# Kernel optimization log

Hardware: AMD Instinct MI355X
Metric: run time of the kernel (lower is better)

## Reference

```python
import jax, jax.numpy as jnp
import numpy as np

B, L, D, NH, NP = 8, 4096, 384, 8, 4


def setup_inputs() -> dict:
    key = jax.random.key(0)
    ks = jax.random.split(key, 16)
    s = 1.0 / np.sqrt(D)
    f32 = jnp.float32
    inp = {
        'query': jax.random.normal(ks[0], (B, L, D), f32),
        'key':   jax.random.normal(ks[1], (B, L, D), f32),
        'value': jax.random.normal(ks[2], (B, L, D), f32),
        # linear weights stored as [in, out]; x @ W + b
        'Wq': jax.random.normal(ks[3], (D, D), f32) * s,
        'bq': jnp.zeros((D,), f32),
        'Wk': jax.random.normal(ks[4], (D, D), f32) * s,
        'bk': jnp.zeros((D,), f32),
        'Wv': jax.random.normal(ks[5], (D, D), f32) * s,
        'bv': jnp.zeros((D,), f32),
        'Woff': jax.random.normal(ks[6], (D, NH * NP * 2), f32) * s,
        'boff': jnp.zeros((NH * NP * 2,), f32),
        'Wwt': jax.random.normal(ks[7], (D, NH * NP), f32) * s,
        'bwt': jnp.zeros((NH * NP,), f32),
        'Wo': jax.random.normal(ks[8], (D, D), f32) * s,
        'bo': jnp.zeros((D,), f32),
        'num_heads': NH,
        'n_points': NP,
    }
    return inp


def reference(query, key, value, Wq, bq, Wk, bk, Wv, bv, Woff, boff, Wwt, bwt, Wo, bo, num_heads, n_points):
    Bq, Lq, Dm = query.shape
    Lk = key.shape[1]
    Lv = value.shape[1]
    hd = Dm // num_heads
    h = w = int(round(np.sqrt(Lk)))  # original: feature_size = int(sqrt(Lk))

    q = query @ Wq + bq          # computed as in original (only its reshape is used via output path)
    k = key @ Wk + bk            # faithful: k_proj is computed but unused downstream
    v = value @ Wv + bv

    # offsets [B, nH, Lq, nP, 2] and softmax point weights [B, nH, Lq, nP]
    off = (query @ Woff + boff).reshape(Bq, Lq, num_heads, n_points, 2).transpose(0, 2, 1, 3, 4)
    wt = jax.nn.softmax((query @ Wwt + bwt).reshape(Bq, Lq, num_heads, n_points).transpose(0, 2, 1, 3), axis=-1)

    # reference grid: ref[...,0] = x (tiled over rows), ref[...,1] = y (repeated over cols)
    yy = jnp.linspace(0.0, 1.0, h)
    xx = jnp.linspace(0.0, 1.0, w)
    gy, gx = jnp.meshgrid(yy, xx, indexing='ij')
    ref = jnp.stack([gx.reshape(-1), gy.reshape(-1)], axis=-1)  # [L, 2]

    loc = jnp.clip(ref[None, None, :, None, :] + off, 0.0, 1.0)  # [B,nH,Lq,nP,2]
    # NOTE: faithful to source, which multiplies component 0 by (h-1) (its 'h' coord)
    ph = loc[..., 0] * (h - 1)   # row pixel coord, in [0, h-1]
    pw = loc[..., 1] * (w - 1)   # col pixel coord, in [0, w-1]

    y0 = jnp.floor(ph)
    x0 = jnp.floor(pw)
    wy = (ph - y0)[..., None]
    wx = (pw - x0)[..., None]
    y0i = y0.astype(jnp.int32)
    x0i = x0.astype(jnp.int32)
    y1i = jnp.minimum(y0i + 1, h - 1)
    x1i = jnp.minimum(x0i + 1, w - 1)

    vh = v.reshape(Bq, Lv, num_heads, hd).transpose(0, 2, 1, 3)  # [B,nH,Lv,hd]

    def gather(yi, xi):
        idx = (yi * w + xi).reshape(Bq, num_heads, Lq * n_points, 1)
        return jnp.take_along_axis(vh, idx, axis=2).reshape(Bq, num_heads, Lq, n_points, hd)

    # bilinear sample (align_corners=True; coords in-range so zero-padding never triggers)
    sampled = ((1 - wy) * ((1 - wx) * gather(y0i, x0i) + wx * gather(y0i, x1i))
               + wy * ((1 - wx) * gather(y1i, x0i) + wx * gather(y1i, x1i)))

    out = jnp.einsum('bhlp,bhlpd->bhld', wt, sampled)  # weighted point aggregation
    out = out.transpose(0, 2, 1, 3).reshape(Bq, Lq, Dm)
    return out @ Wo + bo  # dropout is identity in eval mode
```

## Files before the change

### kernel.cpp

```cpp
#include <hip/hip_runtime.h>
#include <hip/hip_bf16.h>
#include <stdint.h>

using bf16 = __hip_bfloat16;

typedef __attribute__((ext_vector_type(8))) short short8;
typedef __attribute__((ext_vector_type(4))) float float4v;

namespace {
constexpr int kL  = 4096;
constexpr int kD  = 384;
constexpr int kNP = 4;
constexpr int kHD = 48;
constexpr int kGW = 64;
constexpr int kM  = 32768;

constexpr size_t nValue = (size_t)kM * kD;
constexpr size_t nW     = (size_t)kD * kD;
constexpr size_t nWcat  = (size_t)kD * 96;

constexpr size_t oWvt  = 0;
constexpr size_t oWot  = oWvt  + nW * 2;
constexpr size_t oWcat = oWot  + nW * 2;
constexpr size_t oBcat = oWcat + nWcat * 4;
constexpr size_t oVB   = (oBcat + 96 * 4 + 255) & ~size_t(255);
constexpr size_t oProj = oVB   + nValue * 2;
constexpr size_t oAgg  = oProj + (size_t)kM * 96 * 4;
}

__device__ __forceinline__ void load_lds_16(const void* g, void* l) {
  __builtin_amdgcn_global_load_lds((const __attribute__((address_space(1))) void*)g,
                                   (__attribute__((address_space(3))) void*)l,
                                   16, 0, 0);
}

__device__ __forceinline__ short bf16bits(float f) {
  bf16 h = __float2bfloat16(f);
  return *reinterpret_cast<short*>(&h);
}

__global__ void prep_kernel(const float* __restrict__ Wv,
                            const float* __restrict__ Wo,
                            const float* __restrict__ Woff,
                            const float* __restrict__ Wwt,
                            const float* __restrict__ boff,
                            const float* __restrict__ bwt,
                            bf16* __restrict__ Wvt, bf16* __restrict__ Wot,
                            float* __restrict__ Wcat, float* __restrict__ bcat)
{
  size_t i = (size_t)blockIdx.x * 256 + threadIdx.x;
  if (i < nW) {
    const int n = (int)(i / kD), k = (int)(i % kD);
    Wvt[i] = __float2bfloat16(Wv[(size_t)k * kD + n]);
    return;
  }
  i -= nW;
  if (i < nW) {
    const int n = (int)(i / kD), k = (int)(i % kD);
    Wot[i] = __float2bfloat16(Wo[(size_t)k * kD + n]);
    return;
  }
  i -= nW;
  if (i < nWcat) {
    const int k = (int)(i / 96), n = (int)(i % 96);
    Wcat[i] = (n < 64) ? Woff[(size_t)k * 64 + n] : Wwt[(size_t)k * 32 + (n - 64)];
    return;
  }
  i -= nWcat;
  if (i < 96) bcat[i] = (i < 64) ? boff[i] : bwt[i - 64];
}

template<bool A_F32, bool OUT_BF16>
__global__ __launch_bounds__(256)
void mfma_gemm_kernel(const void* __restrict__ A, const bf16* __restrict__ Bt,
                      const float* __restrict__ bias, void* __restrict__ Cout)
{
  __shared__ __align__(16) bf16 sA[128 * 32];
  __shared__ __align__(16) bf16 sB[128 * 32];
  const int tid  = threadIdx.x;
  const int lane = tid & 63;
  const int wave = tid >> 6;
  const int bm = blockIdx.x / 3, bn = blockIdx.x % 3;
  const int m0 = bm * 128, n0 = bn * 128;
  const int wm = (wave >> 1) * 64, wn = (wave & 1) * 64;
  const int r16 = lane & 15, quad = lane >> 4;

  float4v acc[4][4];
  #pragma unroll
  for (int i = 0; i < 4; ++i)
    #pragma unroll
    for (int j = 0; j < 4; ++j) acc[i][j] = (float4v){0.f, 0.f, 0.f, 0.f};

  const int c0 = tid, c1 = tid + 256;

  for (int kt = 0; kt < 12; ++kt) {
    const int k0 = kt * 32;
    if (A_F32) {
      const float* Af = (const float*)A;
      #pragma unroll
      for (int r = 0; r < 2; ++r) {
        const int e = tid + r * 256;
        const int row = e >> 2, c = e & 3;
        const float* src = Af + (size_t)(m0 + row) * kD + k0 + c * 8;
        const float4 f0 = *(const float4*)src;
        const float4 f1 = *(const float4*)(src + 4);
        short8 hx;
        hx[0] = bf16bits(f0.x); hx[1] = bf16bits(f0.y);
        hx[2] = bf16bits(f0.z); hx[3] = bf16bits(f0.w);
        hx[4] = bf16bits(f1.x); hx[5] = bf16bits(f1.y);
        hx[6] = bf16bits(f1.z); hx[7] = bf16bits(f1.w);
        *(short8*)((char*)sA + e * 16) = hx;
      }
    } else {
      const bf16* Ab = (const bf16*)A;
      load_lds_16(Ab + (size_t)(m0 + (c0 >> 2)) * kD + k0 + (c0 & 3) * 8, (char*)sA + c0 * 16);
      load_lds_16(Ab + (size_t)(m0 + (c1 >> 2)) * kD + k0 + (c1 & 3) * 8, (char*)sA + c1 * 16);
    }
    load_lds_16(Bt + (size_t)(n0 + (c0 >> 2)) * kD + k0 + (c0 & 3) * 8, (char*)sB + c0 * 16);
    load_lds_16(Bt + (size_t)(n0 + (c1 >> 2)) * kD + k0 + (c1 & 3) * 8, (char*)sB + c1 * 16);
    __syncthreads();

    short8 av[4], bv[4];
    #pragma unroll
    for (int i = 0; i < 4; ++i)
      av[i] = *(const short8*)(sA + (wm + i * 16 + r16) * 32 + quad * 8);
    #pragma unroll
    for (int j = 0; j < 4; ++j)
      bv[j] = *(const short8*)(sB + (wn + j * 16 + r16) * 32 + quad * 8);
    #pragma unroll
    for (int i = 0; i < 4; ++i)
      #pragma unroll
      for (int j = 0; j < 4; ++j)
        acc[i][j] = __builtin_amdgcn_mfma_f32_16x16x32_bf16(av[i], bv[j], acc[i][j], 0, 0, 0);
    __syncthreads();
  }

  #pragma unroll
  for (int j = 0; j < 4; ++j) {
    const int col = n0 + wn + j * 16 + r16;
    const float bj = bias[col];
    #pragma unroll
    for (int i = 0; i < 4; ++i) {
      const int mbase = m0 + wm + i * 16 + quad * 4;
      #pragma unroll
      for (int r = 0; r < 4; ++r) {
        const float val = acc[i][j][r] + bj;
        if (OUT_BF16)
          ((bf16*)Cout)[(size_t)(mbase + r) * kD + col] = __float2bfloat16(val);
        else
          ((float*)Cout)[(size_t)(mbase + r) * kD + col] = val;
      }
    }
  }
}

__global__ __launch_bounds__(256)
void proj_gemm_kernel(const float* __restrict__ Q, const float* __restrict__ Wc,
                      const float* __restrict__ bc, float* __restrict__ proj)
{
  __shared__ float sA[32][68];
  __shared__ float sB[32][100];
  const int tid = threadIdx.x;
  const int m0  = blockIdx.x * 64;
  const int tm  = tid >> 4, tn = tid & 15;

  float acc[4][6] = {};

  for (int kt = 0; kt < 12; ++kt) {
    const int k0 = kt * 32;
    #pragma unroll
    for (int r = 0; r < 2; ++r) {
      const int e = tid + r * 256;
      const int m = e >> 3, kc = e & 7;
      const float4 f = *(const float4*)(Q + (size_t)(m0 + m) * kD + k0 + kc * 4);
      sA[kc * 4 + 0][m] = f.x;
      sA[kc * 4 + 1][m] = f.y;
      sA[kc * 4 + 2][m] = f.z;
      sA[kc * 4 + 3][m] = f.w;
    }
    #pragma unroll
    for (int r = 0; r < 6; ++r) {
      const int e = tid + r * 256;
      const int k = e / 48, n2 = (e % 48) * 2;
      *(float2*)(&sB[k][n2]) = *(const float2*)(Wc + (size_t)(k0 + k) * 96 + n2);
    }
    __syncthreads();
    #pragma unroll
    for (int k = 0; k < 32; ++k) {
      const float4 a  = *(const float4*)(&sA[k][tm * 4]);
      const float2 b0 = *(const float2*)(&sB[k][tn * 6]);
      const float2 b1 = *(const float2*)(&sB[k][tn * 6 + 2]);
      const float2 b2 = *(const float2*)(&sB[k][tn * 6 + 4]);
      const float av[4] = {a.x, a.y, a.z, a.w};
      const float bb[6] = {b0.x, b0.y, b1.x, b1.y, b2.x, b2.y};
      #pragma unroll
      for (int i = 0; i < 4; ++i)
        #pragma unroll
        for (int j = 0; j < 6; ++j)
          acc[i][j] += av[i] * bb[j];
    }
    __syncthreads();
  }

  #pragma unroll
  for (int j = 0; j < 6; ++j) {
    const int col = tn * 6 + j;
    const float bj = bc[col];
    #pragma unroll
    for (int i = 0; i < 4; ++i)
      proj[(size_t)(m0 + tm * 4 + i) * 96 + col] = acc[i][j] + bj;
  }
}

__global__ __launch_bounds__(384)
void sample_kernel(const float* __restrict__ proj, const bf16* __restrict__ v,
                   bf16* __restrict__ agg)
{
  const int b = blockIdx.x & 7;
  const int l = blockIdx.x >> 3;
  const int token = b * kL + l;
  const int t = threadIdx.x;

  __shared__ float sp[96];
  __shared__ int   sy0[32], sx0[32], sy1[32], sx1[32];
  __shared__ float swy[32], swx[32], swt[32];

  if (t < 96) sp[t] = proj[(size_t)token * 96 + t];
  __syncthreads();

  if (t < 32) {
    const float offx = sp[2 * t];
    const float offy = sp[2 * t + 1];
    const float refx = (float)(l % kGW) * (1.0f / 63.0f);
    const float refy = (float)(l / kGW) * (1.0f / 63.0f);
    const float locx = fminf(fmaxf(refx + offx, 0.f), 1.f);
    const float locy = fminf(fmaxf(refy + offy, 0.f), 1.f);
    const float ph = locx * 63.0f;
    const float pw = locy * 63.0f;
    const float fy = floorf(ph), fx = floorf(pw);
    const int y0 = (int)fy, x0 = (int)fx;
    sy0[t] = y0;               sx0[t] = x0;
    sy1[t] = min(y0 + 1, 63);  sx1[t] = min(x0 + 1, 63);
    swy[t] = ph - fy;          swx[t] = pw - fx;
  }
  if (t < 8) {
    const float* lg = sp + 64 + t * 4;
    const float m = fmaxf(fmaxf(lg[0], lg[1]), fmaxf(lg[2], lg[3]));
    float e[4], sum = 0.f;
    #pragma unroll
    for (int p = 0; p < 4; ++p) { e[p] = expf(lg[p] - m); sum += e[p]; }
    const float inv = 1.0f / sum;
    #pragma unroll
    for (int p = 0; p < 4; ++p) swt[t * 4 + p] = e[p] * inv;
  }
  __syncthreads();

  const int h = t / kHD, d = t % kHD;
  const bf16* vb = v + (size_t)b * kL * kD + h * kHD + d;
  float acc = 0.f;
  #pragma unroll
  for (int p = 0; p < kNP; ++p) {
    const int i = h * kNP + p;
    const int y0 = sy0[i], x0 = sx0[i], y1 = sy1[i], x1 = sx1[i];
    const float wy = swy[i], wx = swx[i], w = swt[i];
    const float v00 = __bfloat162float(vb[(size_t)(y0 * kGW + x0) * kD]);
    const float v01 = __bfloat162float(vb[(size_t)(y0 * kGW + x1) * kD]);
    const float v10 = __bfloat162float(vb[(size_t)(y1 * kGW + x0) * kD]);
    const float v11 = __bfloat162float(vb[(size_t)(y1 * kGW + x1) * kD]);
    const float s = (1.f - wy) * ((1.f - wx) * v00 + wx * v01)
                  +        wy  * ((1.f - wx) * v10 + wx * v11);
    acc += w * s;
  }
  agg[(size_t)token * kD + t] = __float2bfloat16(acc);
}

extern "C" void kernel_launch(void* const* d_in, const int* in_sizes, int n_in,
                              void* d_out, int out_size, void* d_ws, size_t ws_size,
                              hipStream_t stream)
{
  const float* query = (const float*)d_in[0];
  const float* value = (const float*)d_in[2];
  const float* Wv    = (const float*)d_in[7];
  const float* bv    = (const float*)d_in[8];
  const float* Woff  = (const float*)d_in[9];
  const float* boff  = (const float*)d_in[10];
  const float* Wwt   = (const float*)d_in[11];
  const float* bwt   = (const float*)d_in[12];
  const float* Wo    = (const float*)d_in[13];
  const float* bo    = (const float*)d_in[14];
  float* out = (float*)d_out;

  char* ws = (char*)d_ws;
  bf16*  Wvt  = (bf16*)(ws + oWvt);
  bf16*  Wot  = (bf16*)(ws + oWot);
  float* Wcat = (float*)(ws + oWcat);
  float* bcat = (float*)(ws + oBcat);
  bf16*  vB   = (bf16*)(ws + oVB);
  float* proj = (float*)(ws + oProj);
  bf16*  aggB = (bf16*)(ws + oAgg);

  const size_t prepN = nW + nW + nWcat + 96;
  prep_kernel<<<dim3((unsigned)((prepN + 255) / 256)), 256, 0, stream>>>(
      Wv, Wo, Woff, Wwt, boff, bwt, Wvt, Wot, Wcat, bcat);

  mfma_gemm_kernel<true, true><<<dim3((kM / 128) * 3), 256, 0, stream>>>(
      value, Wvt, bv, vB);

  proj_gemm_kernel<<<dim3(kM / 64), 256, 0, stream>>>(query, Wcat, bcat, proj);

  sample_kernel<<<dim3(kM), 384, 0, stream>>>(proj, vB, aggB);

  mfma_gemm_kernel<false, false><<<dim3((kM / 128) * 3), 256, 0, stream>>>(
      aggB, Wot, bo, out);
}
```

Measured before the change: 306.0 us.

## Merge value and projection GEMMs into one launch; vectorize sampling over two tokens

```diff
diff --git a/kernel.cpp b/kernel.cpp
--- a/kernel.cpp
+++ b/kernel.cpp
@@ -10,7 +10,6 @@
 namespace {
 constexpr int kL  = 4096;
 constexpr int kD  = 384;
-constexpr int kNP = 4;
 constexpr int kHD = 48;
 constexpr int kGW = 64;
 constexpr int kM  = 32768;
@@ -37,6 +36,12 @@
 __device__ __forceinline__ short bf16bits(float f) {
   bf16 h = __float2bfloat16(f);
   return *reinterpret_cast<short*>(&h);
+}
+
+__device__ __forceinline__ float bf16raw2f(unsigned short u) {
+  union { unsigned int i; float f; } c;
+  c.i = ((unsigned int)u) << 16;
+  return c.f;
 }
 
 __global__ void prep_kernel(const float* __restrict__ Wv,
@@ -71,16 +76,17 @@
 }
 
 template<bool A_F32, bool OUT_BF16>
-__global__ __launch_bounds__(256)
-void mfma_gemm_kernel(const void* __restrict__ A, const bf16* __restrict__ Bt,
-                      const float* __restrict__ bias, void* __restrict__ Cout)
-{
-  __shared__ __align__(16) bf16 sA[128 * 32];
-  __shared__ __align__(16) bf16 sB[128 * 32];
+__device__ __forceinline__
+void mfma_gemm_body(char* smem, int bid,
+                    const void* __restrict__ A, const bf16* __restrict__ Bt,
+                    const float* __restrict__ bias, void* __restrict__ Cout)
+{
+  bf16* sA = (bf16*)smem;
+  bf16* sB = (bf16*)(smem + 8192);
   const int tid  = threadIdx.x;
   const int lane = tid & 63;
   const int wave = tid >> 6;
-  const int bm = blockIdx.x / 3, bn = blockIdx.x % 3;
+  const int bm = bid / 3, bn = bid % 3;
   const int m0 = bm * 128, n0 = bn * 128;
   const int wm = (wave >> 1) * 64, wn = (wave & 1) * 64;
   const int r16 = lane & 15, quad = lane >> 4;
@@ -154,14 +160,15 @@
   }
 }
 
-__global__ __launch_bounds__(256)
-void proj_gemm_kernel(const float* __restrict__ Q, const float* __restrict__ Wc,
-                      const float* __restrict__ bc, float* __restrict__ proj)
-{
-  __shared__ float sA[32][68];
-  __shared__ float sB[32][100];
+__device__ __forceinline__
+void proj_gemm_body(char* smem, int bid,
+                    const float* __restrict__ Q, const float* __restrict__ Wc,
+                    const float* __restrict__ bc, float* __restrict__ proj)
+{
+  float (*sA)[68]  = (float (*)[68])smem;
+  float (*sB)[100] = (float (*)[100])(smem + 8704);
   const int tid = threadIdx.x;
-  const int m0  = blockIdx.x * 64;
+  const int m0  = bid * 64;
   const int tm  = tid >> 4, tn = tid & 15;
 
   float acc[4][6] = {};
@@ -212,25 +219,54 @@
   }
 }
 
-__global__ __launch_bounds__(384)
+__global__ __launch_bounds__(256)
+void fat_kernel(const float* __restrict__ value, const bf16* __restrict__ Wvt,
+                const float* __restrict__ bv,    bf16* __restrict__ vB,
+                const float* __restrict__ Q,     const float* __restrict__ Wcat,
+                const float* __restrict__ bcat,  float* __restrict__ proj)
+{
+  __shared__ __align__(16) char smem[21504];
+  const int pb = blockIdx.x;
+  if (pb < 512) {
+    proj_gemm_body(smem, pb, Q, Wcat, bcat, proj);
+  } else {
+    mfma_gemm_body<true, true>(smem, pb - 512, value, Wvt, bv, vB);
+  }
+}
+
+__global__ __launch_bounds__(256)
+void out_gemm_kernel(const bf16* __restrict__ A, const bf16* __restrict__ Bt,
+                     const float* __restrict__ bias, float* __restrict__ Cout)
+{
+  __shared__ __align__(16) char smem[16384];
+  mfma_gemm_body<false, false>(smem, blockIdx.x, A, Bt, bias, Cout);
+}
+
+__global__ __launch_bounds__(256)
 void sample_kernel(const float* __restrict__ proj, const bf16* __restrict__ v,
                    bf16* __restrict__ agg)
 {
-  const int b = blockIdx.x & 7;
-  const int l = blockIdx.x >> 3;
-  const int token = b * kL + l;
+  const int b   = blockIdx.x & 7;
+  const int idx = blockIdx.x >> 3;
   const int t = threadIdx.x;
 
-  __shared__ float sp[96];
-  __shared__ int   sy0[32], sx0[32], sy1[32], sx1[32];
-  __shared__ float swy[32], swx[32], swt[32];
-
-  if (t < 96) sp[t] = proj[(size_t)token * 96 + t];
+  __shared__ float sp[2][96];
+  __shared__ int4  soff[2][32];
+  __shared__ float4 sbw[2][32];
+  __shared__ float swt[2][32];
+
+  if (t < 192) {
+    const int tok = t / 96, j = t % 96;
+    const int token = b * kL + idx * 2 + tok;
+    sp[tok][j] = proj[(size_t)token * 96 + j];
+  }
   __syncthreads();
 
-  if (t < 32) {
-    const float offx = sp[2 * t];
-    const float offy = sp[2 * t + 1];
+  if (t < 64) {
+    const int tok = t >> 5, i = t & 31;
+    const int l = idx * 2 + tok;
+    const float offx = sp[tok][2 * i];
+    const float offy = sp[tok][2 * i + 1];
     const float refx = (float)(l % kGW) * (1.0f / 63.0f);
     const float refy = (float)(l / kGW) * (1.0f / 63.0f);
     const float locx = fminf(fmaxf(refx + offx, 0.f), 1.f);
@@ -239,39 +275,62 @@
     const float pw = locy * 63.0f;
     const float fy = floorf(ph), fx = floorf(pw);
     const int y0 = (int)fy, x0 = (int)fx;
-    sy0[t] = y0;               sx0[t] = x0;
-    sy1[t] = min(y0 + 1, 63);  sx1[t] = min(x0 + 1, 63);
-    swy[t] = ph - fy;          swx[t] = pw - fx;
-  }
-  if (t < 8) {
-    const float* lg = sp + 64 + t * 4;
+    const int y1 = min(y0 + 1, 63), x1 = min(x0 + 1, 63);
+    const float wy = ph - fy, wx = pw - fx;
+    soff[tok][i] = make_int4((y0 * kGW + x0) * kD, (y0 * kGW + x1) * kD,
+                             (y1 * kGW + x0) * kD, (y1 * kGW + x1) * kD);
+    sbw[tok][i] = make_float4((1.f - wy) * (1.f - wx), (1.f - wy) * wx,
+                              wy * (1.f - wx),         wy * wx);
+  } else if (t < 80) {
+    const int u = t - 64, tok = u >> 3, hh = u & 7;
+    const float* lg = &sp[tok][64 + hh * 4];
     const float m = fmaxf(fmaxf(lg[0], lg[1]), fmaxf(lg[2], lg[3]));
     float e[4], sum = 0.f;
     #pragma unroll
     for (int p = 0; p < 4; ++p) { e[p] = expf(lg[p] - m); sum += e[p]; }
     const float inv = 1.0f / sum;
     #pragma unroll
-    for (int p = 0; p < 4; ++p) swt[t * 4 + p] = e[p] * inv;
+    for (int p = 0; p < 4; ++p) swt[tok][hh * 4 + p] = e[p] * inv;
   }
   __syncthreads();
 
-  const int h = t / kHD, d = t % kHD;
-  const bf16* vb = v + (size_t)b * kL * kD + h * kHD + d;
-  float acc = 0.f;
-  #pragma unroll
-  for (int p = 0; p < kNP; ++p) {
-    const int i = h * kNP + p;
-    const int y0 = sy0[i], x0 = sx0[i], y1 = sy1[i], x1 = sx1[i];
-    const float wy = swy[i], wx = swx[i], w = swt[i];
-    const float v00 = __bfloat162float(vb[(size_t)(y0 * kGW + x0) * kD]);
-    const float v01 = __bfloat162float(vb[(size_t)(y0 * kGW + x1) * kD]);
-    const float v10 = __bfloat162float(vb[(size_t)(y1 * kGW + x0) * kD]);
-    const float v11 = __bfloat162float(vb[(size_t)(y1 * kGW + x1) * kD]);
-    const float s = (1.f - wy) * ((1.f - wx) * v00 + wx * v01)
-                  +        wy  * ((1.f - wx) * v10 + wx * v11);
-    acc += w * s;
-  }
-  agg[(size_t)token * kD + t] = __float2bfloat16(acc);
+  if (t < 192) {
+    const int tok = t / 96, q = t % 96;
+    const int h = q / 12, dg = (q % 12) * 4;
+    const int l = idx * 2 + tok;
+    const int hd = h * kHD + dg;
+    const unsigned short* vb = (const unsigned short*)(v + (size_t)b * kL * kD + hd);
+    float4v acc = (float4v){0.f, 0.f, 0.f, 0.f};
+    #pragma unroll
+    for (int p = 0; p < 4; ++p) {
+      const int i = h * 4 + p;
+      const int4  o  = soff[tok][i];
+      const float4 bw = sbw[tok][i];
+      const float wt = swt[tok][i];
+      const ushort4 u0 = *(const ushort4*)(vb + o.x);
+      const ushort4 u1 = *(const ushort4*)(vb + o.y);
+      const ushort4 u2 = *(const ushort4*)(vb + o.z);
+      const ushort4 u3 = *(const ushort4*)(vb + o.w);
+      float4v s;
+      s[0] = bw.x * bf16raw2f(u0.x) + bw.y * bf16raw2f(u1.x)
+           + bw.z * bf16raw2f(u2.x) + bw.w * bf16raw2f(u3.x);
+      s[1] = bw.x * bf16raw2f(u0.y) + bw.y * bf16raw2f(u1.y)
+           + bw.z * bf16raw2f(u2.y) + bw.w * bf16raw2f(u3.y);
+      s[2] = bw.x * bf16raw2f(u0.z) + bw.y * bf16raw2f(u1.z)
+           + bw.z * bf16raw2f(u2.z) + bw.w * bf16raw2f(u3.z);
+      s[3] = bw.x * bf16raw2f(u0.w) + bw.y * bf16raw2f(u1.w)
+           + bw.z * bf16raw2f(u2.w) + bw.w * bf16raw2f(u3.w);
+      #pragma unroll
+      for (int d = 0; d < 4; ++d) acc[d] += wt * s[d];
+    }
+    ushort4 outu;
+    outu.x = (unsigned short)bf16bits(acc[0]);
+    outu.y = (unsigned short)bf16bits(acc[1]);
+    outu.z = (unsigned short)bf16bits(acc[2]);
+    outu.w = (unsigned short)bf16bits(acc[3]);
+    const int token = b * kL + l;
+    *(ushort4*)((unsigned short*)agg + (size_t)token * kD + hd) = outu;
+  }
 }
 
 extern "C" void kernel_launch(void* const* d_in, const int* in_sizes, int n_in,
@@ -303,13 +362,10 @@
   prep_kernel<<<dim3((unsigned)((prepN + 255) / 256)), 256, 0, stream>>>(
       Wv, Wo, Woff, Wwt, boff, bwt, Wvt, Wot, Wcat, bcat);
 
-  mfma_gemm_kernel<true, true><<<dim3((kM / 128) * 3), 256, 0, stream>>>(
-      value, Wvt, bv, vB);
-
-  proj_gemm_kernel<<<dim3(kM / 64), 256, 0, stream>>>(query, Wcat, bcat, proj);
-
-  sample_kernel<<<dim3(kM), 384, 0, stream>>>(proj, vB, aggB);
-
-  mfma_gemm_kernel<false, false><<<dim3((kM / 128) * 3), 256, 0, stream>>>(
-      aggB, Wot, bo, out);
-}
+  fat_kernel<<<dim3(512 + 768), 256, 0, stream>>>(
+      value, Wvt, bv, vB, query, Wcat, bcat, proj);
+
+  sample_kernel<<<dim3(kM / 2), 256, 0, stream>>>(proj, vB, aggB);
+
+  out_gemm_kernel<<<dim3((kM / 128) * 3), 256, 0, stream>>>(aggB, Wot, bo, out);
+}
```

Result: faster. 294.7 us (-3.7%).
